# Kernel optimization log

Measured on AMD Instinct MI355X. Metric: run time of the kernel, lower is better.

The kernel has to match this reference:

```python
import jax, jax.numpy as jnp
import numpy as np

STRIDE = 1
PADDING = 1


def setup_inputs() -> dict:
    key = jax.random.key(0)
    k1, k2 = jax.random.split(key)
    x = jax.random.normal(k1, (32, 64, 112, 112), dtype=jnp.float32)
    weights = jax.random.normal(k2, (128, 64, 3, 3), dtype=jnp.float32)
    biases = jnp.zeros((128,), dtype=jnp.float32)
    return {"x": x, "weights": weights, "biases": biases}


def reference(x, weights, biases):
    # NCHW input, OIHW weights -> NCHW output; zero padding, stride 1.
    out = jax.lax.conv_general_dilated(
        x, weights,
        window_strides=(STRIDE, STRIDE),
        padding=((PADDING, PADDING), (PADDING, PADDING)),
        dimension_numbers=("NCHW", "OIHW", "NCHW"),
    )
    return out + biases[None, :, None, None]
```

## Files before the change

kernel.cpp:

```cpp
#include <hip/hip_runtime.h>
#include <stdint.h>

typedef unsigned short u16;
typedef __attribute__((ext_vector_type(8))) short bf16x8;
typedef __attribute__((ext_vector_type(4))) float f32x4;

#define C_IN    64
#define K_OUT   128
#define HW      112
#define HW2     (HW * HW)
#define CP      72
#define NW      114
#define THREADS 256

__device__ __forceinline__ u16 f2bf(float f) {
  union { float f; uint32_t u; } x; x.f = f;
  return (u16)((x.u + 0x7FFFu + ((x.u >> 16) & 1u)) >> 16);
}

__global__ void prep_weights(const float* __restrict__ w, u16* __restrict__ wt) {
  int idx = blockIdx.x * 256 + threadIdx.x;
  if (idx >= K_OUT * C_IN * 9) return;
  int c    = idx & (C_IN - 1);
  int kout = (idx >> 6) & (K_OUT - 1);
  int rs   = idx >> 13;
  wt[idx] = f2bf(w[(kout * C_IN + c) * 9 + rs]);
}

__global__ __launch_bounds__(THREADS, 3) void conv3x3(
    const float* __restrict__ x, const u16* __restrict__ wt,
    const float* __restrict__ bias, float* __restrict__ out) {
  __shared__ u16 Xs[3][NW][CP];

  const int tid = threadIdx.x;

  const int bid = blockIdx.x;
  const int lb  = (bid & 7) * 448 + (bid >> 3);
  const int n = lb / HW;
  const int h = lb % HW;

  if (tid < 192) {
    const int seg  = tid >> 5;
    const int cd   = (tid & 31) * 2;
    const int r    = seg >> 1;
    const int wcol = (seg & 1) ? (NW - 1) : 0;
    *(uint32_t*)&Xs[r][wcol][cd] = 0u;
  }
  if (h == 0) {
    for (int t = tid; t < NW * 32; t += THREADS)
      *(uint32_t*)&Xs[0][t >> 5][(t & 31) * 2] = 0u;
  } else if (h == HW - 1) {
    for (int t = tid; t < NW * 32; t += THREADS)
      *(uint32_t*)&Xs[2][t >> 5][(t & 31) * 2] = 0u;
  }

  const float* xn = x + (size_t)n * C_IN * HW2;
  for (int it = 0; it < 11; ++it) {
    const int task = tid + it * THREADS;
    if (task < 3 * 28 * 32) {
      const int cp   = task & 31;
      const int rest = task >> 5;
      const int w4   = rest % 28;
      const int r    = rest / 28;
      const int row  = h + r - 1;
      if (row >= 0 && row < HW) {
        const float* xrow = xn + (size_t)(2 * cp) * HW2 + (size_t)row * HW + w4 * 4;
        const float4 va = *(const float4*)(xrow);
        const float4 vb = *(const float4*)(xrow + HW2);
        const int wb = 1 + w4 * 4;
        const int c  = 2 * cp;
        *(uint32_t*)&Xs[r][wb + 0][c] = (uint32_t)f2bf(va.x) | ((uint32_t)f2bf(vb.x) << 16);
        *(uint32_t*)&Xs[r][wb + 1][c] = (uint32_t)f2bf(va.y) | ((uint32_t)f2bf(vb.y) << 16);
        *(uint32_t*)&Xs[r][wb + 2][c] = (uint32_t)f2bf(va.z) | ((uint32_t)f2bf(vb.z) << 16);
        *(uint32_t*)&Xs[r][wb + 3][c] = (uint32_t)f2bf(va.w) | ((uint32_t)f2bf(vb.w) << 16);
      }
    }
  }

  __syncthreads();

  const int lane = tid & 63;
  const int wave = tid >> 6;
  const int quad = lane >> 4;
  const int l15  = lane & 15;
  const int kb   = wave * 32;

  f32x4 acc[2][7];
#pragma unroll
  for (int i = 0; i < 2; ++i)
#pragma unroll
    for (int j = 0; j < 7; ++j) acc[i][j] = (f32x4){0.f, 0.f, 0.f, 0.f};

#pragma unroll
  for (int rs = 0; rs < 9; ++rs) {
    const int r = rs / 3;
    const int s = rs % 3;
    const u16* wbase = wt + rs * (K_OUT * C_IN);
#pragma unroll
    for (int ch = 0; ch < 2; ++ch) {
      const int c0 = ch * 32 + quad * 8;
      const bf16x8 a0 = *(const bf16x8*)(wbase + (kb + l15) * C_IN + c0);
      const bf16x8 a1 = *(const bf16x8*)(wbase + (kb + 16 + l15) * C_IN + c0);
#pragma unroll
      for (int w7 = 0; w7 < 7; ++w7) {
        const bf16x8 b = *(const bf16x8*)&Xs[r][w7 * 16 + l15 + s][c0];
        acc[0][w7] = __builtin_amdgcn_mfma_f32_16x16x32_bf16(a0, b, acc[0][w7], 0, 0, 0);
        acc[1][w7] = __builtin_amdgcn_mfma_f32_16x16x32_bf16(a1, b, acc[1][w7], 0, 0, 0);
      }
    }
  }

  float* on = out + (size_t)n * K_OUT * HW2 + (size_t)h * HW;
#pragma unroll
  for (int mt = 0; mt < 2; ++mt) {
#pragma unroll
    for (int rg = 0; rg < 4; ++rg) {
      const int kout = kb + mt * 16 + quad * 4 + rg;
      const float bv = bias[kout];
      float* orow = on + (size_t)kout * HW2;
#pragma unroll
      for (int w7 = 0; w7 < 7; ++w7) {
        orow[w7 * 16 + l15] = acc[mt][w7][rg] + bv;
      }
    }
  }
}

extern "C" void kernel_launch(void* const* d_in, const int* in_sizes, int n_in,
                              void* d_out, int out_size, void* d_ws, size_t ws_size,
                              hipStream_t stream) {
  const float* x  = (const float*)d_in[0];
  const float* w  = (const float*)d_in[1];
  const float* bi = (const float*)d_in[2];
  float* out = (float*)d_out;
  u16* wt = (u16*)d_ws;

  prep_weights<<<(K_OUT * C_IN * 9 + 255) / 256, 256, 0, stream>>>(w, wt);
  conv3x3<<<32 * HW, THREADS, 0, stream>>>(x, wt, bi, out);
}
```

Measured before the change: 378.4 us.

## Split input channels into two halves to halve LDS and raise occupancy

The shared input tile now holds only 32 channels (36 padded), loaded and consumed in two passes over channel halves. This halves LDS per block and raises the launch bound target from 3 to 6 blocks per CU, aiming to hide global load latency across more resident blocks. Weight fragments are software-prefetched one filter tap ahead, and the tap loop is no longer unrolled. The cost is an extra barrier round, serialized load-then-compute phases within each block, and register pressure under the tighter launch bound.

After: 484.7 us. 28.1% more time.

```diff
diff --git a/kernel.cpp b/kernel.cpp
--- a/kernel.cpp
+++ b/kernel.cpp
@@ -9,7 +9,7 @@
 #define K_OUT   128
 #define HW      112
 #define HW2     (HW * HW)
-#define CP      72
+#define CPH     36
 #define NW      114
 #define THREADS 256
 
@@ -27,10 +27,10 @@
   wt[idx] = f2bf(w[(kout * C_IN + c) * 9 + rs]);
 }
 
-__global__ __launch_bounds__(THREADS, 3) void conv3x3(
+__global__ __launch_bounds__(THREADS, 6) void conv3x3(
     const float* __restrict__ x, const u16* __restrict__ wt,
     const float* __restrict__ bias, float* __restrict__ out) {
-  __shared__ u16 Xs[3][NW][CP];
+  __shared__ u16 Xs[3][NW][CPH];
 
   const int tid = threadIdx.x;
 
@@ -39,45 +39,20 @@
   const int n = lb / HW;
   const int h = lb % HW;
 
-  if (tid < 192) {
-    const int seg  = tid >> 5;
-    const int cd   = (tid & 31) * 2;
+  if (tid < 96) {
+    const int seg  = tid >> 4;
+    const int cd   = (tid & 15) * 2;
     const int r    = seg >> 1;
     const int wcol = (seg & 1) ? (NW - 1) : 0;
     *(uint32_t*)&Xs[r][wcol][cd] = 0u;
   }
   if (h == 0) {
-    for (int t = tid; t < NW * 32; t += THREADS)
-      *(uint32_t*)&Xs[0][t >> 5][(t & 31) * 2] = 0u;
+    uint32_t* p = (uint32_t*)&Xs[0][0][0];
+    for (int t = tid; t < NW * (CPH / 2); t += THREADS) p[t] = 0u;
   } else if (h == HW - 1) {
-    for (int t = tid; t < NW * 32; t += THREADS)
-      *(uint32_t*)&Xs[2][t >> 5][(t & 31) * 2] = 0u;
+    uint32_t* p = (uint32_t*)&Xs[2][0][0];
+    for (int t = tid; t < NW * (CPH / 2); t += THREADS) p[t] = 0u;
   }
-
-  const float* xn = x + (size_t)n * C_IN * HW2;
-  for (int it = 0; it < 11; ++it) {
-    const int task = tid + it * THREADS;
-    if (task < 3 * 28 * 32) {
-      const int cp   = task & 31;
-      const int rest = task >> 5;
-      const int w4   = rest % 28;
-      const int r    = rest / 28;
-      const int row  = h + r - 1;
-      if (row >= 0 && row < HW) {
-        const float* xrow = xn + (size_t)(2 * cp) * HW2 + (size_t)row * HW + w4 * 4;
-        const float4 va = *(const float4*)(xrow);
-        const float4 vb = *(const float4*)(xrow + HW2);
-        const int wb = 1 + w4 * 4;
-        const int c  = 2 * cp;
-        *(uint32_t*)&Xs[r][wb + 0][c] = (uint32_t)f2bf(va.x) | ((uint32_t)f2bf(vb.x) << 16);
-        *(uint32_t*)&Xs[r][wb + 1][c] = (uint32_t)f2bf(va.y) | ((uint32_t)f2bf(vb.y) << 16);
-        *(uint32_t*)&Xs[r][wb + 2][c] = (uint32_t)f2bf(va.z) | ((uint32_t)f2bf(vb.z) << 16);
-        *(uint32_t*)&Xs[r][wb + 3][c] = (uint32_t)f2bf(va.w) | ((uint32_t)f2bf(vb.w) << 16);
-      }
-    }
-  }
-
-  __syncthreads();
 
   const int lane = tid & 63;
   const int wave = tid >> 6;
@@ -91,23 +66,60 @@
 #pragma unroll
     for (int j = 0; j < 7; ++j) acc[i][j] = (f32x4){0.f, 0.f, 0.f, 0.f};
 
-#pragma unroll
-  for (int rs = 0; rs < 9; ++rs) {
-    const int r = rs / 3;
-    const int s = rs % 3;
-    const u16* wbase = wt + rs * (K_OUT * C_IN);
-#pragma unroll
-    for (int ch = 0; ch < 2; ++ch) {
-      const int c0 = ch * 32 + quad * 8;
-      const bf16x8 a0 = *(const bf16x8*)(wbase + (kb + l15) * C_IN + c0);
-      const bf16x8 a1 = *(const bf16x8*)(wbase + (kb + 16 + l15) * C_IN + c0);
-#pragma unroll
-      for (int w7 = 0; w7 < 7; ++w7) {
-        const bf16x8 b = *(const bf16x8*)&Xs[r][w7 * 16 + l15 + s][c0];
-        acc[0][w7] = __builtin_amdgcn_mfma_f32_16x16x32_bf16(a0, b, acc[0][w7], 0, 0, 0);
-        acc[1][w7] = __builtin_amdgcn_mfma_f32_16x16x32_bf16(a1, b, acc[1][w7], 0, 0, 0);
+  const float* xn = x + (size_t)n * C_IN * HW2;
+
+  for (int chalf = 0; chalf < 2; ++chalf) {
+    {
+      const float* xh = xn + (size_t)(chalf * 32) * HW2;
+#pragma unroll 1
+      for (int it = 0; it < 6; ++it) {
+        const int task = tid + it * THREADS;
+        if (task < 3 * 28 * 16) {
+          const int cp   = task & 15;
+          const int rest = task >> 4;
+          const int w4   = rest % 28;
+          const int r    = rest / 28;
+          const int row  = h + r - 1;
+          if (row >= 0 && row < HW) {
+            const float* xrow = xh + (size_t)(2 * cp) * HW2 + (size_t)row * HW + w4 * 4;
+            const float4 va = *(const float4*)(xrow);
+            const float4 vb = *(const float4*)(xrow + HW2);
+            const int wb = 1 + w4 * 4;
+            const int c  = 2 * cp;
+            *(uint32_t*)&Xs[r][wb + 0][c] = (uint32_t)f2bf(va.x) | ((uint32_t)f2bf(vb.x) << 16);
+            *(uint32_t*)&Xs[r][wb + 1][c] = (uint32_t)f2bf(va.y) | ((uint32_t)f2bf(vb.y) << 16);
+            *(uint32_t*)&Xs[r][wb + 2][c] = (uint32_t)f2bf(va.z) | ((uint32_t)f2bf(vb.z) << 16);
+            *(uint32_t*)&Xs[r][wb + 3][c] = (uint32_t)f2bf(va.w) | ((uint32_t)f2bf(vb.w) << 16);
+          }
+        }
       }
     }
+    __syncthreads();
+
+    {
+      const int cof = chalf * 32 + quad * 8;
+      const u16* w0p = wt + (size_t)(kb + l15) * C_IN + cof;
+      const u16* w1p = wt + (size_t)(kb + 16 + l15) * C_IN + cof;
+      bf16x8 a0 = *(const bf16x8*)(w0p);
+      bf16x8 a1 = *(const bf16x8*)(w1p);
+#pragma unroll 1
+      for (int rs = 0; rs < 9; ++rs) {
+        const int nrs = (rs < 8) ? rs + 1 : 8;
+        const bf16x8 na0 = *(const bf16x8*)(w0p + nrs * (K_OUT * C_IN));
+        const bf16x8 na1 = *(const bf16x8*)(w1p + nrs * (K_OUT * C_IN));
+        const int r = rs / 3;
+        const int s = rs - r * 3;
+        const u16* xrow = &Xs[r][l15 + s][quad * 8];
+#pragma unroll
+        for (int w7 = 0; w7 < 7; ++w7) {
+          const bf16x8 b = *(const bf16x8*)(xrow + w7 * 16 * CPH);
+          acc[0][w7] = __builtin_amdgcn_mfma_f32_16x16x32_bf16(a0, b, acc[0][w7], 0, 0, 0);
+          acc[1][w7] = __builtin_amdgcn_mfma_f32_16x16x32_bf16(a1, b, acc[1][w7], 0, 0, 0);
+        }
+        a0 = na0; a1 = na1;
+      }
+    }
+    if (chalf == 0) __syncthreads();
   }
 
   float* on = out + (size_t)n * K_OUT * HW2 + (size_t)h * HW;
```

## Split output width across two wave groups with 512-thread blocks

Applied to the files above, without the earlier changes.

Doubles the block to 8 waves, with waves 0-3 computing output column tiles 0-3 and waves 4-7 computing tiles 4-6 for the same output channels. The shared-memory staging loop now takes fewer iterations per thread and is unrolled. The aim is more waves resident per CU and fewer accumulators per wave to hide load latency. The cost is that each weight fragment is now loaded by two waves, and the 4-vs-3 tile split leaves the two wave groups with unequal work.

New measurement: 429.8 us. 1.14x slower.

```diff
diff --git a/kernel.cpp b/kernel.cpp
--- a/kernel.cpp
+++ b/kernel.cpp
@@ -11,7 +11,7 @@
 #define HW2     (HW * HW)
 #define CP      72
 #define NW      114
-#define THREADS 256
+#define THREADS 512
 
 __device__ __forceinline__ u16 f2bf(float f) {
   union { float f; uint32_t u; } x; x.f = f;
@@ -27,7 +27,54 @@
   wt[idx] = f2bf(w[(kout * C_IN + c) * 9 + rs]);
 }
 
-__global__ __launch_bounds__(THREADS, 3) void conv3x3(
+template <int WLO, int WN>
+__device__ __forceinline__ void do_tile(
+    const u16 (&Xs)[3][NW][CP], const u16* __restrict__ wt,
+    const float* __restrict__ bias, float* __restrict__ out,
+    int n, int h, int kb, int quad, int l15) {
+  f32x4 acc[2][WN];
+#pragma unroll
+  for (int i = 0; i < 2; ++i)
+#pragma unroll
+    for (int j = 0; j < WN; ++j) acc[i][j] = (f32x4){0.f, 0.f, 0.f, 0.f};
+
+#pragma unroll
+  for (int rs = 0; rs < 9; ++rs) {
+    const int r = rs / 3;
+    const int s = rs - r * 3;
+    const u16* wbase = wt + rs * (K_OUT * C_IN);
+#pragma unroll
+    for (int ch = 0; ch < 2; ++ch) {
+      const int c0 = ch * 32 + quad * 8;
+      const bf16x8 a0 = *(const bf16x8*)(wbase + (kb + l15) * C_IN + c0);
+      const bf16x8 a1 = *(const bf16x8*)(wbase + (kb + 16 + l15) * C_IN + c0);
+#pragma unroll
+      for (int j = 0; j < WN; ++j) {
+        const int w7 = WLO + j;
+        const bf16x8 b = *(const bf16x8*)&Xs[r][w7 * 16 + l15 + s][c0];
+        acc[0][j] = __builtin_amdgcn_mfma_f32_16x16x32_bf16(a0, b, acc[0][j], 0, 0, 0);
+        acc[1][j] = __builtin_amdgcn_mfma_f32_16x16x32_bf16(a1, b, acc[1][j], 0, 0, 0);
+      }
+    }
+  }
+
+  float* on = out + (size_t)n * K_OUT * HW2 + (size_t)h * HW;
+#pragma unroll
+  for (int mt = 0; mt < 2; ++mt) {
+#pragma unroll
+    for (int rg = 0; rg < 4; ++rg) {
+      const int kout = kb + mt * 16 + quad * 4 + rg;
+      const float bv = bias[kout];
+      float* orow = on + (size_t)kout * HW2;
+#pragma unroll
+      for (int j = 0; j < WN; ++j) {
+        orow[(WLO + j) * 16 + l15] = acc[mt][j][rg] + bv;
+      }
+    }
+  }
+}
+
+__global__ __launch_bounds__(THREADS, 6) void conv3x3(
     const float* __restrict__ x, const u16* __restrict__ wt,
     const float* __restrict__ bias, float* __restrict__ out) {
   __shared__ u16 Xs[3][NW][CP];
@@ -55,7 +102,8 @@
   }
 
   const float* xn = x + (size_t)n * C_IN * HW2;
-  for (int it = 0; it < 11; ++it) {
+#pragma unroll
+  for (int it = 0; it < 6; ++it) {
     const int task = tid + it * THREADS;
     if (task < 3 * 28 * 32) {
       const int cp   = task & 31;
@@ -83,46 +131,13 @@
   const int wave = tid >> 6;
   const int quad = lane >> 4;
   const int l15  = lane & 15;
-  const int kb   = wave * 32;
+  const int kb   = (wave & 3) * 32;
+  const int wh   = wave >> 2;
 
-  f32x4 acc[2][7];
-#pragma unroll
-  for (int i = 0; i < 2; ++i)
-#pragma unroll
-    for (int j = 0; j < 7; ++j) acc[i][j] = (f32x4){0.f, 0.f, 0.f, 0.f};
-
-#pragma unroll
-  for (int rs = 0; rs < 9; ++rs) {
-    const int r = rs / 3;
-    const int s = rs % 3;
-    const u16* wbase = wt + rs * (K_OUT * C_IN);
-#pragma unroll
-    for (int ch = 0; ch < 2; ++ch) {
-      const int c0 = ch * 32 + quad * 8;
-      const bf16x8 a0 = *(const bf16x8*)(wbase + (kb + l15) * C_IN + c0);
-      const bf16x8 a1 = *(const bf16x8*)(wbase + (kb + 16 + l15) * C_IN + c0);
-#pragma unroll
-      for (int w7 = 0; w7 < 7; ++w7) {
-        const bf16x8 b = *(const bf16x8*)&Xs[r][w7 * 16 + l15 + s][c0];
-        acc[0][w7] = __builtin_amdgcn_mfma_f32_16x16x32_bf16(a0, b, acc[0][w7], 0, 0, 0);
-        acc[1][w7] = __builtin_amdgcn_mfma_f32_16x16x32_bf16(a1, b, acc[1][w7], 0, 0, 0);
-      }
-    }
-  }
-
-  float* on = out + (size_t)n * K_OUT * HW2 + (size_t)h * HW;
-#pragma unroll
-  for (int mt = 0; mt < 2; ++mt) {
-#pragma unroll
-    for (int rg = 0; rg < 4; ++rg) {
-      const int kout = kb + mt * 16 + quad * 4 + rg;
-      const float bv = bias[kout];
-      float* orow = on + (size_t)kout * HW2;
-#pragma unroll
-      for (int w7 = 0; w7 < 7; ++w7) {
-        orow[w7 * 16 + l15] = acc[mt][w7][rg] + bv;
-      }
-    }
+  if (wh == 0) {
+    do_tile<0, 4>(Xs, wt, bias, out, n, h, kb, quad, l15);
+  } else {
+    do_tile<4, 3>(Xs, wt, bias, out, n, h, kb, quad, l15);
   }
 }
 
```

## Reorder conv loop to channel-outer, prefetch weights and double-buffer LDS fragments

Applied to the files above, without the earlier changes.

Swaps the loop nest so the channel half is outermost. For each half, all nine tap weight fragments are loaded into registers up front, and the next tap's LDS B fragments are prefetched while the current MFMAs run. Occupancy is relaxed from 3 to 2 blocks per SIMD to leave room for the extra registers, and the staging loop is fully unrolled. The aim is to hide global and LDS latency behind MFMA issue, at the cost of higher register pressure and fewer resident waves.

Result: no change. 377.7 us (-0.2%).

```diff
diff --git a/kernel.cpp b/kernel.cpp
--- a/kernel.cpp
+++ b/kernel.cpp
@@ -27,7 +27,7 @@
   wt[idx] = f2bf(w[(kout * C_IN + c) * 9 + rs]);
 }
 
-__global__ __launch_bounds__(THREADS, 3) void conv3x3(
+__global__ __launch_bounds__(THREADS, 2) void conv3x3(
     const float* __restrict__ x, const u16* __restrict__ wt,
     const float* __restrict__ bias, float* __restrict__ out) {
   __shared__ u16 Xs[3][NW][CP];
@@ -55,6 +55,7 @@
   }
 
   const float* xn = x + (size_t)n * C_IN * HW2;
+#pragma unroll
   for (int it = 0; it < 11; ++it) {
     const int task = tid + it * THREADS;
     if (task < 3 * 28 * 32) {
@@ -92,20 +93,41 @@
     for (int j = 0; j < 7; ++j) acc[i][j] = (f32x4){0.f, 0.f, 0.f, 0.f};
 
 #pragma unroll
-  for (int rs = 0; rs < 9; ++rs) {
-    const int r = rs / 3;
-    const int s = rs % 3;
-    const u16* wbase = wt + rs * (K_OUT * C_IN);
+  for (int ch = 0; ch < 2; ++ch) {
+    const int c0 = ch * 32 + quad * 8;
+    const u16* xb = &Xs[0][l15][c0];
+    const u16* wp = wt + (size_t)(kb + l15) * C_IN + c0;
+
+    bf16x8 A0[9], A1[9];
 #pragma unroll
-    for (int ch = 0; ch < 2; ++ch) {
-      const int c0 = ch * 32 + quad * 8;
-      const bf16x8 a0 = *(const bf16x8*)(wbase + (kb + l15) * C_IN + c0);
-      const bf16x8 a1 = *(const bf16x8*)(wbase + (kb + 16 + l15) * C_IN + c0);
+    for (int rs = 0; rs < 9; ++rs) {
+      A0[rs] = *(const bf16x8*)(wp + rs * (K_OUT * C_IN));
+      A1[rs] = *(const bf16x8*)(wp + rs * (K_OUT * C_IN) + 16 * C_IN);
+    }
+
+    bf16x8 B[7];
+#pragma unroll
+    for (int w7 = 0; w7 < 7; ++w7)
+      B[w7] = *(const bf16x8*)(xb + (w7 * 16) * CP);
+
+#pragma unroll
+    for (int rs = 0; rs < 9; ++rs) {
+      bf16x8 Bn[7];
+      if (rs < 8) {
+        const int r1 = (rs + 1) / 3;
+        const int s1 = (rs + 1) - r1 * 3;
+#pragma unroll
+        for (int w7 = 0; w7 < 7; ++w7)
+          Bn[w7] = *(const bf16x8*)(xb + (r1 * NW + s1 + w7 * 16) * CP);
+      }
 #pragma unroll
       for (int w7 = 0; w7 < 7; ++w7) {
-        const bf16x8 b = *(const bf16x8*)&Xs[r][w7 * 16 + l15 + s][c0];
-        acc[0][w7] = __builtin_amdgcn_mfma_f32_16x16x32_bf16(a0, b, acc[0][w7], 0, 0, 0);
-        acc[1][w7] = __builtin_amdgcn_mfma_f32_16x16x32_bf16(a1, b, acc[1][w7], 0, 0, 0);
+        acc[0][w7] = __builtin_amdgcn_mfma_f32_16x16x32_bf16(A0[rs], B[w7], acc[0][w7], 0, 0, 0);
+        acc[1][w7] = __builtin_amdgcn_mfma_f32_16x16x32_bf16(A1[rs], B[w7], acc[1][w7], 0, 0, 0);
+      }
+      if (rs < 8) {
+#pragma unroll
+        for (int w7 = 0; w7 < 7; ++w7) B[w7] = Bn[w7];
       }
     }
   }
```
